# Performance work log

Hardware: AMD Instinct MI355X
Metric: run time of the kernel (lower is better)

## Reference

```python
import jax, jax.numpy as jnp
import numpy as np


def setup_inputs() -> dict:
    key = jax.random.key(0)
    x = jax.random.normal(key, (8, 48, 48, 48, 64), dtype=jnp.float32)
    gamma = jnp.float32(1e-4)  # matches tf.Variable(0.0001)
    return {"x": x, "gamma": gamma}


def reference(x, gamma):
    # x: (B, W, D, H, C)
    B, W, D, H, C = x.shape
    N = W * D * H
    # Keras Reshape((C, -1)) is a row-major flatten of (W, D, H, C) -> (C, N).
    # NOTE: this is NOT a channels-first transpose; it is a raw reshape,
    # exactly as the original module computes it.
    K = x.reshape(B, C, N)                      # (B, C, N)
    # Q = K^T and J = K^T in the original, so m1 = K@Q and m2 = K@J are both
    # the same Gram matrix G = K @ K^T. Compute it once.
    G = jnp.einsum('bcn,bdn->bcd', K, K)        # (B, C, C)
    m3 = jnp.einsum('bcd,bde->bce', G, G)       # (B, C, C)
    affinity = jax.nn.sigmoid(m3)               # (B, C, C)
    weights = jnp.einsum('bcd,bdn->bcn', affinity, K)  # (B, C, N)
    weights = weights.reshape(B, W, D, H, C)
    return gamma * weights + x
```

## Files before the change

kernel.cpp:

```cpp
#include <hip/hip_runtime.h>

#define NCOL 110592
#define NCH  64
#define CN   (NCOL * NCH)
#define NB   8

typedef __attribute__((ext_vector_type(8))) __bf16 bf16x8;
typedef __attribute__((ext_vector_type(4))) float  f32x4;

__global__ __launch_bounds__(256) void k_gram(const float* __restrict__ x,
                                              float* __restrict__ part,
                                              int steps) {
    const int b     = blockIdx.y;
    const int chunk = blockIdx.x;
    const int tid   = threadIdx.x;
    const int w     = tid >> 6;
    const int lane  = tid & 63;
    const int r     = lane & 15;
    const int q     = lane >> 4;

    const float* xb = x + (size_t)b * CN;

    f32x4 acc0 = {0.f, 0.f, 0.f, 0.f};
    f32x4 acc1 = {0.f, 0.f, 0.f, 0.f};
    f32x4 acc2 = {0.f, 0.f, 0.f, 0.f};
    f32x4 acc3 = {0.f, 0.f, 0.f, 0.f};

    const int kbase = chunk * steps * 32 + q * 8;

    for (int s = 0; s < steps; ++s) {
        const int k0 = kbase + s * 32;
        bf16x8 frag[4];
#pragma unroll
        for (int i = 0; i < 4; ++i) {
            const float* p = xb + (i * 16 + r) * NCOL + k0;
            f32x4 lo = *(const f32x4*)p;
            f32x4 hi = *(const f32x4*)(p + 4);
            bf16x8 f;
            f[0] = (__bf16)lo[0]; f[1] = (__bf16)lo[1];
            f[2] = (__bf16)lo[2]; f[3] = (__bf16)lo[3];
            f[4] = (__bf16)hi[0]; f[5] = (__bf16)hi[1];
            f[6] = (__bf16)hi[2]; f[7] = (__bf16)hi[3];
            frag[i] = f;
        }
        bf16x8 af = (w == 0) ? frag[0] : (w == 1) ? frag[1]
                  : (w == 2) ? frag[2] : frag[3];
        acc0 = __builtin_amdgcn_mfma_f32_16x16x32_bf16(af, frag[0], acc0, 0, 0, 0);
        acc1 = __builtin_amdgcn_mfma_f32_16x16x32_bf16(af, frag[1], acc1, 0, 0, 0);
        acc2 = __builtin_amdgcn_mfma_f32_16x16x32_bf16(af, frag[2], acc2, 0, 0, 0);
        acc3 = __builtin_amdgcn_mfma_f32_16x16x32_bf16(af, frag[3], acc3, 0, 0, 0);
    }

    float* pp = part + (size_t)(b * gridDim.x + chunk) * 4096;
#pragma unroll
    for (int rr = 0; rr < 4; ++rr) {
        const int m = w * 16 + q * 4 + rr;
        pp[m * 64 + (0 * 16 + r)] = acc0[rr];
        pp[m * 64 + (1 * 16 + r)] = acc1[rr];
        pp[m * 64 + (2 * 16 + r)] = acc2[rr];
        pp[m * 64 + (3 * 16 + r)] = acc3[rr];
    }
}

__global__ __launch_bounds__(256) void k_reduce(const float* __restrict__ part,
                                                float* __restrict__ G,
                                                int chunks) {
    const int b    = blockIdx.y;
    const int cell = blockIdx.x * 512 + threadIdx.x;
    float s0 = 0.f, s1 = 0.f;
    for (int p = 0; p < chunks; ++p) {
        const float* pp = part + (size_t)(b * chunks + p) * 4096;
        s0 += pp[cell];
        s1 += pp[cell + 256];
    }
    G[b * 4096 + cell]       = s0;
    G[b * 4096 + cell + 256] = s1;
}

__global__ __launch_bounds__(256) void k_affinity(const float* __restrict__ G,
                                                  const float* __restrict__ gptr,
                                                  float* __restrict__ A) {
    const int b = blockIdx.x;
    __shared__ float Gs[64 * 65];
    const float* Gb = G + b * 4096;
    for (int i = threadIdx.x; i < 4096; i += 256)
        Gs[(i >> 6) * 65 + (i & 63)] = Gb[i];
    __syncthreads();
    const float gamma = gptr[0];
    for (int id = threadIdx.x; id < 4096; id += 256) {
        const int c = id >> 6, e = id & 63;
        float dot = 0.f;
#pragma unroll
        for (int d = 0; d < 64; ++d)
            dot += Gs[c * 65 + d] * Gs[e * 65 + d];
        const float aff = 1.0f / (1.0f + __expf(-dot));
        A[b * 4096 + id] = gamma * aff + ((c == e) ? 1.0f : 0.0f);
    }
}

__global__ __launch_bounds__(256) void k_apply(const float* __restrict__ x,
                                               const float* __restrict__ A,
                                               float* __restrict__ out) {
    const int b  = blockIdx.y;
    const int n0 = blockIdx.x * 512 + threadIdx.x;
    const float* xb = x + (size_t)b * CN;
    float*       ob = out + (size_t)b * CN;
    const float* Ab = A + b * 4096;

    float acc0[64], acc1[64];
#pragma unroll
    for (int c = 0; c < 64; ++c) { acc0[c] = 0.f; acc1[c] = 0.f; }

#pragma unroll 4
    for (int d = 0; d < 64; ++d) {
        const float k0 = xb[d * NCOL + n0];
        const float k1 = xb[d * NCOL + n0 + 256];
#pragma unroll
        for (int c = 0; c < 64; ++c) {
            const float a = Ab[d * 64 + c];
            acc0[c] += a * k0;
            acc1[c] += a * k1;
        }
    }

#pragma unroll
    for (int c = 0; c < 64; ++c) {
        ob[c * NCOL + n0]       = acc0[c];
        ob[c * NCOL + n0 + 256] = acc1[c];
    }
}

extern "C" void kernel_launch(void* const* d_in, const int* in_sizes, int n_in,
                              void* d_out, int out_size, void* d_ws, size_t ws_size,
                              hipStream_t stream) {
    const float* x    = (const float*)d_in[0];
    const float* gptr = (const float*)d_in[1];
    float*       out  = (float*)d_out;
    float*       ws   = (float*)d_ws;

    int chunks = 64;
    auto need = [](int ch) { return (size_t)(8 * ch + 16) * 4096 * 4; };
    if (ws_size < need(64)) chunks = 32;
    if (ws_size < need(32)) chunks = 8;
    if (ws_size < need(8))  chunks = 2;
    const int steps = 3456 / chunks;

    float* part = ws;
    float* G    = ws + (size_t)8 * chunks * 4096;
    float* Aff  = G + 8 * 4096;

    k_gram    <<<dim3(chunks, 8), 256, 0, stream>>>(x, part, steps);
    k_reduce  <<<dim3(8, 8),      256, 0, stream>>>(part, G, chunks);
    k_affinity<<<8,               256, 0, stream>>>(G, gptr, Aff);
    k_apply   <<<dim3(216, 8),    256, 0, stream>>>(x, Aff, out);
}
```

Before: 531.9 us.

## Vectorize reduce/apply memory access and double gram chunk count

The gram kernel now gets 128 chunks per batch when workspace allows, so more blocks run in parallel on the dominant read of x. The reduce kernel splits the chunk sum across four thread groups with float4 loads and a shared-memory combine, and the affinity loader uses float4 reads. The apply kernel has each thread handle two adjacent columns with float2 loads and stores instead of two strided scalars. Together these aim to improve bandwidth use and parallelism, at the cost of more partial-sum traffic and possibly different register pressure in apply.

```diff
diff --git a/kernel.cpp b/kernel.cpp
--- a/kernel.cpp
+++ b/kernel.cpp
@@ -33,7 +33,7 @@
         bf16x8 frag[4];
 #pragma unroll
         for (int i = 0; i < 4; ++i) {
-            const float* p = xb + (i * 16 + r) * NCOL + k0;
+            const float* p = xb + (size_t)(i * 16 + r) * NCOL + k0;
             f32x4 lo = *(const f32x4*)p;
             f32x4 hi = *(const f32x4*)(p + 4);
             bf16x8 f;
@@ -66,15 +66,29 @@
                                                 float* __restrict__ G,
                                                 int chunks) {
     const int b    = blockIdx.y;
-    const int cell = blockIdx.x * 512 + threadIdx.x;
-    float s0 = 0.f, s1 = 0.f;
-    for (int p = 0; p < chunks; ++p) {
-        const float* pp = part + (size_t)(b * chunks + p) * 4096;
-        s0 += pp[cell];
-        s1 += pp[cell + 256];
+    const int cq   = threadIdx.x & 63;
+    const int ph   = threadIdx.x >> 6;
+    const int cell = blockIdx.x * 256 + cq * 4;
+
+    f32x4 s = {0.f, 0.f, 0.f, 0.f};
+    for (int p = ph; p < chunks; p += 4) {
+        const f32x4 v = *(const f32x4*)(part + (size_t)(b * chunks + p) * 4096 + cell);
+        s[0] += v[0]; s[1] += v[1]; s[2] += v[2]; s[3] += v[3];
     }
-    G[b * 4096 + cell]       = s0;
-    G[b * 4096 + cell + 256] = s1;
+
+    __shared__ f32x4 red[4][64];
+    red[ph][cq] = s;
+    __syncthreads();
+    if (ph == 0) {
+        const f32x4 a = red[0][cq], b1 = red[1][cq];
+        const f32x4 c = red[2][cq], d = red[3][cq];
+        f32x4 o;
+        o[0] = a[0] + b1[0] + c[0] + d[0];
+        o[1] = a[1] + b1[1] + c[1] + d[1];
+        o[2] = a[2] + b1[2] + c[2] + d[2];
+        o[3] = a[3] + b1[3] + c[3] + d[3];
+        *(f32x4*)(G + b * 4096 + cell) = o;
+    }
 }
 
 __global__ __launch_bounds__(256) void k_affinity(const float* __restrict__ G,
@@ -83,8 +97,15 @@
     const int b = blockIdx.x;
     __shared__ float Gs[64 * 65];
     const float* Gb = G + b * 4096;
-    for (int i = threadIdx.x; i < 4096; i += 256)
-        Gs[(i >> 6) * 65 + (i & 63)] = Gb[i];
+    for (int i = threadIdx.x; i < 1024; i += 256) {
+        const f32x4 v = *(const f32x4*)(Gb + i * 4);
+        const int row = i >> 4;
+        const int col = (i & 15) * 4;
+        Gs[row * 65 + col + 0] = v[0];
+        Gs[row * 65 + col + 1] = v[1];
+        Gs[row * 65 + col + 2] = v[2];
+        Gs[row * 65 + col + 3] = v[3];
+    }
     __syncthreads();
     const float gamma = gptr[0];
     for (int id = threadIdx.x; id < 4096; id += 256) {
@@ -102,32 +123,29 @@
                                                const float* __restrict__ A,
                                                float* __restrict__ out) {
     const int b  = blockIdx.y;
-    const int n0 = blockIdx.x * 512 + threadIdx.x;
+    const int n0 = (blockIdx.x * 256 + threadIdx.x) * 2;
     const float* xb = x + (size_t)b * CN;
     float*       ob = out + (size_t)b * CN;
     const float* Ab = A + b * 4096;
 
-    float acc0[64], acc1[64];
+    float2 acc[64];
 #pragma unroll
-    for (int c = 0; c < 64; ++c) { acc0[c] = 0.f; acc1[c] = 0.f; }
+    for (int c = 0; c < 64; ++c) { acc[c].x = 0.f; acc[c].y = 0.f; }
 
 #pragma unroll 4
     for (int d = 0; d < 64; ++d) {
-        const float k0 = xb[d * NCOL + n0];
-        const float k1 = xb[d * NCOL + n0 + 256];
+        const float2 k = *(const float2*)(xb + (size_t)d * NCOL + n0);
 #pragma unroll
         for (int c = 0; c < 64; ++c) {
             const float a = Ab[d * 64 + c];
-            acc0[c] += a * k0;
-            acc1[c] += a * k1;
+            acc[c].x += a * k.x;
+            acc[c].y += a * k.y;
         }
     }
 
 #pragma unroll
-    for (int c = 0; c < 64; ++c) {
-        ob[c * NCOL + n0]       = acc0[c];
-        ob[c * NCOL + n0 + 256] = acc1[c];
-    }
+    for (int c = 0; c < 64; ++c)
+        *(float2*)(ob + (size_t)c * NCOL + n0) = acc[c];
 }
 
 extern "C" void kernel_launch(void* const* d_in, const int* in_sizes, int n_in,
@@ -138,11 +156,12 @@
     float*       out  = (float*)d_out;
     float*       ws   = (float*)d_ws;
 
-    int chunks = 64;
+    int chunks = 128;
     auto need = [](int ch) { return (size_t)(8 * ch + 16) * 4096 * 4; };
-    if (ws_size < need(64)) chunks = 32;
-    if (ws_size < need(32)) chunks = 8;
-    if (ws_size < need(8))  chunks = 2;
+    if (ws_size < need(128)) chunks = 64;
+    if (ws_size < need(64))  chunks = 32;
+    if (ws_size < need(32))  chunks = 8;
+    if (ws_size < need(8))   chunks = 2;
     const int steps = 3456 / chunks;
 
     float* part = ws;
@@ -150,7 +169,7 @@
     float* Aff  = G + 8 * 4096;
 
     k_gram    <<<dim3(chunks, 8), 256, 0, stream>>>(x, part, steps);
-    k_reduce  <<<dim3(8, 8),      256, 0, stream>>>(part, G, chunks);
+    k_reduce  <<<dim3(16, 8),     256, 0, stream>>>(part, G, chunks);
     k_affinity<<<8,               256, 0, stream>>>(G, gptr, Aff);
     k_apply   <<<dim3(216, 8),    256, 0, stream>>>(x, Aff, out);
 }
```

After: 591.6 us. 1.11x slower.
